# Performance work log

Measured on AMD Instinct MI355X. Metric: run time of the kernel, lower is better.

## Reference

```python
import jax, jax.numpy as jnp
import numpy as np

N_DRUG = 25000
N_DIS = 25000
N = N_DRUG + N_DIS
E = 800000
D_IN = 128
D_OUT = 128


def setup_inputs() -> dict:
    key = jax.random.key(0)
    k1, k2, k3, k4, k5, k6 = jax.random.split(key, 6)
    drug_f = jax.random.normal(k1, (N_DRUG, D_IN), dtype=jnp.float32)
    disease_f = jax.random.normal(k2, (N_DIS, D_IN), dtype=jnp.float32)
    rows = jax.random.randint(k3, (E,), 0, N, dtype=jnp.int64)
    cols = jax.random.randint(k4, (E,), 0, N, dtype=jnp.int64)
    # xavier_uniform_ equivalent for [D_IN, D_OUT]
    limit = float(np.sqrt(6.0 / (D_IN + D_OUT)))
    drug_w = jax.random.uniform(k5, (D_IN, D_OUT), minval=-limit, maxval=limit, dtype=jnp.float32)
    disease_w = jax.random.uniform(k6, (D_IN, D_OUT), minval=-limit, maxval=limit, dtype=jnp.float32)
    return {"drug_f": drug_f, "disease_f": disease_f, "drug_w": drug_w,
            "disease_w": disease_w, "rows": rows, "cols": cols}


def reference(drug_f, disease_f, drug_w, disease_w, rows, cols):
    # per-type linear projection
    drug_h = drug_f @ drug_w          # [n_drug, D_OUT]
    dis_h = disease_f @ disease_w     # [n_dis,  D_OUT]
    node_f = jnp.concatenate([drug_h, dis_h], axis=0)  # [N, D_OUT]
    # row-sum degrees of the (unit-valued) sparse adjacency, clamped at 1
    deg = jax.ops.segment_sum(jnp.ones((rows.shape[0],), node_f.dtype), rows,
                              num_segments=N)
    norm = jnp.clip(deg, 1.0, None) ** -0.5           # [N]
    # symmetric norm: norm * (A @ (norm * x)); SpMM as gather + segment_sum
    node_f = node_f * norm[:, None]
    msgs = node_f[cols]                               # [E, D_OUT]
    node_f = jax.ops.segment_sum(msgs, rows, num_segments=N)
    node_f = node_f * norm[:, None]
    return node_f
```

## Files before the change

kernel.cpp:

```cpp
#include <hip/hip_runtime.h>
#include <hip/hip_bf16.h>

#define D 128
#define CAP 64
#define NSHARD 8
#define NCHUNK 384
#define PART_EDGES 4096

typedef short short8 __attribute__((ext_vector_type(8)));
typedef unsigned short ushort8 __attribute__((ext_vector_type(8)));
typedef float f32x4  __attribute__((ext_vector_type(4)));

__device__ __forceinline__ short f2bf(float x) {
    __hip_bfloat16 b = __float2bfloat16(x);
    return *reinterpret_cast<short*>(&b);
}
__device__ __forceinline__ float bf2f(unsigned short u) {
    return __uint_as_float((unsigned)u << 16);
}

__device__ __forceinline__ void wprep_block(int b16, int tid,
                                            const float* __restrict__ w0,
                                            const float* __restrict__ w1,
                                            __hip_bfloat16* __restrict__ wb) {
    int gid = b16 * 256 + tid;
    int type = gid >> 11;
    int tri  = gid & 2047;
    int lane = tri & 63;
    int ts   = tri >> 6;
    int s = ts & 3, t = ts >> 2;
    const float* W = type ? w1 : w0;
    int n = t * 16 + (lane & 15);
    int kbase = s * 32 + (lane >> 4) * 8;
    short8 v;
    #pragma unroll
    for (int j = 0; j < 8; ++j)
        v[j] = f2bf(W[(size_t)(kbase + j) * D + n]);
    *(short8*)&wb[(size_t)type * 16384 + (size_t)tri * 8] = v;
}

__global__ __launch_bounds__(256) void prep_sort_kernel(const float* __restrict__ w0,
                                                        const float* __restrict__ w1,
                                                        __hip_bfloat16* __restrict__ wb,
                                                        int* __restrict__ bincur, int nbin) {
    int b = blockIdx.x;
    if (b < 16) { wprep_block(b, threadIdx.x, w0, w1, wb); return; }
    int i = threadIdx.x;
    if (i < nbin) bincur[i] = 0;
}

__global__ __launch_bounds__(256) void part_proj_kernel(
    const int* __restrict__ rows, const int* __restrict__ cols,
    int* __restrict__ bincur, unsigned int* __restrict__ payload,
    int E, int nbin, int capbin, int nparts,
    const float* __restrict__ f0, const float* __restrict__ f1,
    const __hip_bfloat16* __restrict__ wb,
    __hip_bfloat16* __restrict__ h,
    int n0, int n1, int nb0) {

    __shared__ short8 Wl[2048];
    int b = blockIdx.x;
    int t = threadIdx.x;

    if (b < nparts) {
        int* hist = (int*)&Wl[0];
        int* base = hist + 256;
        int* cur  = hist + 512;
        int lo = b * PART_EDGES;
        int hi = lo + PART_EDGES; if (hi > E) hi = E;

        hist[t] = 0;
        __syncthreads();
        for (int i = lo + t; i < hi; i += 256)
            atomicAdd(&hist[rows[i] >> 8], 1);
        __syncthreads();
        int c = hist[t];
        base[t] = (t < nbin && c > 0) ? atomicAdd(&bincur[t], c) : 0;
        cur[t] = 0;
        __syncthreads();
        for (int i = lo + t; i < hi; i += 256) {
            int r = rows[i];
            int bn = r >> 8;
            int p = base[bn] + atomicAdd(&cur[bn], 1);
            if (p < capbin)
                payload[(size_t)bn * capbin + p] = ((unsigned)r << 16) | (unsigned)(cols[i] & 0xffff);
        }
        return;
    }

    int pb = b - nparts;
    int type = (pb >= nb0) ? 1 : 0;
    const float* f = type ? f1 : f0;
    int lbase = (type ? (pb - nb0) : pb) * 64;
    int nloc  = type ? n1 : n0;
    int goff  = type ? n0 : 0;

    const short8* src = (const short8*)wb + (size_t)type * 2048;
    for (int i = t; i < 2048; i += 256) Wl[i] = src[i];
    __syncthreads();

    int wave = t >> 6;
    int lane = t & 63;
    int m  = lane & 15;
    int kg = lane >> 4;
    int wrow = lbase + wave * 16;

    int arow = wrow + m;
    int arc = (arow < nloc) ? arow : (nloc - 1);
    const float* fr = f + (size_t)arc * D + kg * 8;
    short8 A[4];
    #pragma unroll
    for (int s = 0; s < 4; ++s) {
        float4 x = *(const float4*)(fr + s * 32);
        float4 y = *(const float4*)(fr + s * 32 + 4);
        short8 a;
        a[0] = f2bf(x.x); a[1] = f2bf(x.y); a[2] = f2bf(x.z); a[3] = f2bf(x.w);
        a[4] = f2bf(y.x); a[5] = f2bf(y.y); a[6] = f2bf(y.z); a[7] = f2bf(y.w);
        A[s] = a;
    }

    #pragma unroll
    for (int tt = 0; tt < 8; ++tt) {
        f32x4 acc = {0.f, 0.f, 0.f, 0.f};
        #pragma unroll
        for (int s = 0; s < 4; ++s)
            acc = __builtin_amdgcn_mfma_f32_16x16x32_bf16(A[s], Wl[(tt * 4 + s) * 64 + lane], acc, 0, 0, 0);
        #pragma unroll
        for (int r = 0; r < 4; ++r) {
            int grow = wrow + kg * 4 + r;
            if (grow < nloc)
                h[(size_t)(goff + grow) * D + tt * 16 + m] = __float2bfloat16(acc[r]);
        }
    }
}

__global__ __launch_bounds__(256) void binfill_kernel(const unsigned int* __restrict__ payload,
                                                      const int* __restrict__ bincur,
                                                      unsigned short* __restrict__ bucket,
                                                      int* __restrict__ cnt,
                                                      float* __restrict__ normf,
                                                      int capbin, int N) {
    __shared__ int rc[256];
    int b = blockIdx.x;
    int t = threadIdx.x;
    rc[t] = 0;
    __syncthreads();
    int cntb = bincur[b]; if (cntb > capbin) cntb = capbin;
    const unsigned int* pp = payload + (size_t)b * capbin;
    for (int i = t; i < cntb; i += 256) {
        unsigned pay = pp[i];
        int rl = (pay >> 16) & 255;
        int p = atomicAdd(&rc[rl], 1);
        if (p < CAP)
            bucket[(size_t)((b << 8) | rl) * CAP + p] = (unsigned short)(pay & 0xffff);
    }
    __syncthreads();
    int r = (b << 8) | t;
    if (r < N) {
        int c = rc[t];
        cnt[r] = c;
        normf[r] = rsqrtf((float)(c < 1 ? 1 : c));
    }
}

__global__ __launch_bounds__(256) void agg_kernel(const int* __restrict__ cnt,
                                                  const float* __restrict__ normf,
                                                  const unsigned short* __restrict__ bucket,
                                                  const __hip_bfloat16* __restrict__ h,
                                                  float* __restrict__ out, int n) {
    int wave = threadIdx.x >> 6;
    int lane = threadIdx.x & 63;
    int r = blockIdx.x * 4 + wave;
    if (r >= n) return;
    int d = cnt[r]; if (d > CAP) d = CAP;
    int s = r * CAP;
    int g  = lane >> 4;
    int sl = lane & 15;

    float acc[8] = {0.f,0.f,0.f,0.f,0.f,0.f,0.f,0.f};
    for (int j = 0; j < d; j += 8) {
        int j0 = j + g, j1 = j + 4 + g;
        bool v0 = j0 < d, v1 = j1 < d;
        int c0 = bucket[s + (v0 ? j0 : 0)];
        int c1 = bucket[s + (v1 ? j1 : 0)];
        float w0 = v0 ? normf[c0] : 0.f;
        float w1 = v1 ? normf[c1] : 0.f;
        ushort8 a = *(const ushort8*)&h[(size_t)c0 * D + sl * 8];
        ushort8 bb = *(const ushort8*)&h[(size_t)c1 * D + sl * 8];
        #pragma unroll
        for (int k = 0; k < 8; ++k)
            acc[k] += w0 * bf2f(a[k]) + w1 * bf2f(bb[k]);
    }
    #pragma unroll
    for (int k = 0; k < 8; ++k) {
        acc[k] += __shfl_xor(acc[k], 16);
        acc[k] += __shfl_xor(acc[k], 32);
    }
    if (g == 0) {
        float nr = normf[r];
        float* po = &out[(size_t)r * D + sl * 8];
        float4 o0 = make_float4(acc[0]*nr, acc[1]*nr, acc[2]*nr, acc[3]*nr);
        float4 o1 = make_float4(acc[4]*nr, acc[5]*nr, acc[6]*nr, acc[7]*nr);
        *(float4*)po = o0;
        *(float4*)(po + 4) = o1;
    }
}

__global__ __launch_bounds__(256) void prep_kernel(const float* __restrict__ w0,
                                                   const float* __restrict__ w1,
                                                   __hip_bfloat16* __restrict__ wb,
                                                   int* __restrict__ cnt, int N) {
    int b = blockIdx.x;
    if (b < 16) { wprep_block(b, threadIdx.x, w0, w1, wb); }
    else {
        int i = (b - 16) * 256 + threadIdx.x;
        if (i < N) cnt[i] = 0;
    }
}

__global__ __launch_bounds__(256) void fill_shard_kernel(const int* __restrict__ rows,
                                                         const int* __restrict__ cols,
                                                         int* __restrict__ cnt,
                                                         unsigned short* __restrict__ bucket,
                                                         int E, int shsz, int ch) {
    int s     = blockIdx.x & (NSHARD - 1);
    int chunk = blockIdx.x >> 3;
    int lo = chunk * ch;
    int hi = lo + ch; if (hi > E) hi = E;
    int rlo = s * shsz;
    for (int i = lo + (int)threadIdx.x; i < hi; i += 256) {
        int r = rows[i];
        if ((unsigned)(r - rlo) < (unsigned)shsz) {
            int p = atomicAdd(&cnt[r], 1);
            if (p < CAP) bucket[(size_t)r * CAP + p] = (unsigned short)cols[i];
        }
    }
}

__global__ void norm_from_cnt_kernel(const int* __restrict__ cnt, float* __restrict__ normf, int N) {
    int i = blockIdx.x * 256 + threadIdx.x;
    if (i < N) { int c = cnt[i]; normf[i] = rsqrtf((float)(c < 1 ? 1 : c)); }
}

extern "C" void kernel_launch(void* const* d_in, const int* in_sizes, int n_in,
                              void* d_out, int out_size, void* d_ws, size_t ws_size,
                              hipStream_t stream) {
    const float* drug_f    = (const float*)d_in[0];
    const float* disease_f = (const float*)d_in[1];
    const float* drug_w    = (const float*)d_in[2];
    const float* disease_w = (const float*)d_in[3];
    const int*   rows      = (const int*)d_in[4];
    const int*   cols      = (const int*)d_in[5];
    float* out = (float*)d_out;

    int n_drug = in_sizes[0] / D;
    int n_dis  = in_sizes[1] / D;
    int N = n_drug + n_dis;
    int E = in_sizes[4];
    (void)out_size; (void)n_in;

    char* ws = (char*)d_ws;
    size_t off = 0;
    auto alloc = [&](size_t bytes) { void* p = ws + off; off = (off + bytes + 255) & ~(size_t)255; return p; };

    int*            cnt      = (int*)alloc(sizeof(int) * N);
    float*          normf    = (float*)alloc(sizeof(float) * N);
    __hip_bfloat16* h_raw    = (__hip_bfloat16*)alloc(sizeof(__hip_bfloat16) * (size_t)N * D);
    __hip_bfloat16* wb       = (__hip_bfloat16*)alloc(sizeof(__hip_bfloat16) * 2 * 16384);
    unsigned short* bucket   = (unsigned short*)alloc((size_t)N * CAP * sizeof(unsigned short));

    int nb0 = (n_drug + 63) / 64;
    int nb1 = (n_dis + 63) / 64;

    int nbin   = (N + 255) >> 8;
    int capbin = (((E / nbin) * 3 / 2) + 63) & ~63;
    size_t sort_need = off
        + ((sizeof(int) * nbin + 255) & ~(size_t)255)
        + ((sizeof(unsigned int) * (size_t)nbin * capbin + 255) & ~(size_t)255);

    if (ws_size >= sort_need && nbin <= 256) {
        int*          bincur  = (int*)alloc(sizeof(int) * nbin);
        unsigned int* payload = (unsigned int*)alloc(sizeof(unsigned int) * (size_t)nbin * capbin);

        int nparts = (E + PART_EDGES - 1) / PART_EDGES;
        prep_sort_kernel<<<17, 256, 0, stream>>>(drug_w, disease_w, wb, bincur, nbin);
        part_proj_kernel<<<nparts + nb0 + nb1, 256, 0, stream>>>(
            rows, cols, bincur, payload, E, nbin, capbin, nparts,
            drug_f, disease_f, wb, h_raw, n_drug, n_dis, nb0);
        binfill_kernel<<<nbin, 256, 0, stream>>>(payload, bincur, bucket, cnt, normf, capbin, N);
        agg_kernel<<<(N + 3) / 4, 256, 0, stream>>>(cnt, normf, bucket, h_raw, out, N);
    } else {
        int shsz = (N + NSHARD - 1) / NSHARD;
        int ch   = (E + NCHUNK - 1) / NCHUNK;
        int prep_blocks = 16 + (N + 255) / 256;

        prep_kernel<<<prep_blocks, 256, 0, stream>>>(drug_w, disease_w, wb, cnt, N);
        fill_shard_kernel<<<NCHUNK * NSHARD, 256, 0, stream>>>(rows, cols, cnt, bucket, E, shsz, ch);
        norm_from_cnt_kernel<<<(N + 255) / 256, 256, 0, stream>>>(cnt, normf, N);
        part_proj_kernel<<<nb0 + nb1, 256, 0, stream>>>(
            rows, cols, (int*)nullptr, (unsigned int*)nullptr, E, nbin, capbin, 0,
            drug_f, disease_f, wb, h_raw, n_drug, n_dis, nb0);
        agg_kernel<<<(N + 3) / 4, 256, 0, stream>>>(cnt, normf, bucket, h_raw, out, N);
    }
}
```

Measured before the change: 78.26 us.

## Halve sort bin width and preload bucket columns per lane in aggregation

Bins in the edge partition/binfill pass now cover 128 rows instead of 256. This doubles the bin count, so binfill runs about twice as many blocks for better GPU occupancy, and the partition kernel's histogram loops are generalised beyond 256 bins. The aggregation kernel now loads each row's column list and neighbour norms once per lane, then broadcasts them with shuffles. It handles one edge per 16-lane group per iteration instead of two, which removes the repeated bucket and norm loads but leaves fewer gathers in flight per iteration.

Result: faster. 71.17 us (-9.1%).

```diff
diff --git a/kernel.cpp b/kernel.cpp
--- a/kernel.cpp
+++ b/kernel.cpp
@@ -3,6 +3,7 @@
 
 #define D 128
 #define CAP 64
+#define BINSH 7
 #define NSHARD 8
 #define NCHUNK 384
 #define PART_EDGES 4096
@@ -45,8 +46,7 @@
                                                         int* __restrict__ bincur, int nbin) {
     int b = blockIdx.x;
     if (b < 16) { wprep_block(b, threadIdx.x, w0, w1, wb); return; }
-    int i = threadIdx.x;
-    if (i < nbin) bincur[i] = 0;
+    for (int i = threadIdx.x; i < nbin; i += 256) bincur[i] = 0;
 }
 
 __global__ __launch_bounds__(256) void part_proj_kernel(
@@ -64,23 +64,25 @@
 
     if (b < nparts) {
         int* hist = (int*)&Wl[0];
-        int* base = hist + 256;
-        int* cur  = hist + 512;
+        int* base = hist + 512;
+        int* cur  = hist + 1024;
         int lo = b * PART_EDGES;
         int hi = lo + PART_EDGES; if (hi > E) hi = E;
 
-        hist[t] = 0;
+        for (int i = t; i < nbin; i += 256) hist[i] = 0;
         __syncthreads();
         for (int i = lo + t; i < hi; i += 256)
-            atomicAdd(&hist[rows[i] >> 8], 1);
+            atomicAdd(&hist[rows[i] >> BINSH], 1);
         __syncthreads();
-        int c = hist[t];
-        base[t] = (t < nbin && c > 0) ? atomicAdd(&bincur[t], c) : 0;
-        cur[t] = 0;
+        for (int i = t; i < nbin; i += 256) {
+            int c = hist[i];
+            base[i] = (c > 0) ? atomicAdd(&bincur[i], c) : 0;
+            cur[i] = 0;
+        }
         __syncthreads();
         for (int i = lo + t; i < hi; i += 256) {
             int r = rows[i];
-            int bn = r >> 8;
+            int bn = r >> BINSH;
             int p = base[bn] + atomicAdd(&cur[bn], 1);
             if (p < capbin)
                 payload[(size_t)bn * capbin + p] = ((unsigned)r << 16) | (unsigned)(cols[i] & 0xffff);
@@ -140,26 +142,28 @@
                                                       int* __restrict__ cnt,
                                                       float* __restrict__ normf,
                                                       int capbin, int N) {
-    __shared__ int rc[256];
+    __shared__ int rc[128];
     int b = blockIdx.x;
     int t = threadIdx.x;
-    rc[t] = 0;
+    if (t < 128) rc[t] = 0;
     __syncthreads();
     int cntb = bincur[b]; if (cntb > capbin) cntb = capbin;
     const unsigned int* pp = payload + (size_t)b * capbin;
     for (int i = t; i < cntb; i += 256) {
         unsigned pay = pp[i];
-        int rl = (pay >> 16) & 255;
+        int rl = (pay >> 16) & 127;
         int p = atomicAdd(&rc[rl], 1);
         if (p < CAP)
-            bucket[(size_t)((b << 8) | rl) * CAP + p] = (unsigned short)(pay & 0xffff);
+            bucket[(size_t)((b << BINSH) | rl) * CAP + p] = (unsigned short)(pay & 0xffff);
     }
     __syncthreads();
-    int r = (b << 8) | t;
-    if (r < N) {
-        int c = rc[t];
-        cnt[r] = c;
-        normf[r] = rsqrtf((float)(c < 1 ? 1 : c));
+    if (t < 128) {
+        int r = (b << BINSH) | t;
+        if (r < N) {
+            int c = rc[t];
+            cnt[r] = c;
+            normf[r] = rsqrtf((float)(c < 1 ? 1 : c));
+        }
     }
 }
 
@@ -174,22 +178,23 @@
     if (r >= n) return;
     int d = cnt[r]; if (d > CAP) d = CAP;
     int s = r * CAP;
+
+    int col = (int)bucket[s + lane];
+    int cs  = (lane < d) ? col : 0;
+    float wl = (lane < d) ? normf[cs] : 0.f;
+
     int g  = lane >> 4;
     int sl = lane & 15;
 
     float acc[8] = {0.f,0.f,0.f,0.f,0.f,0.f,0.f,0.f};
-    for (int j = 0; j < d; j += 8) {
-        int j0 = j + g, j1 = j + 4 + g;
-        bool v0 = j0 < d, v1 = j1 < d;
-        int c0 = bucket[s + (v0 ? j0 : 0)];
-        int c1 = bucket[s + (v1 ? j1 : 0)];
-        float w0 = v0 ? normf[c0] : 0.f;
-        float w1 = v1 ? normf[c1] : 0.f;
-        ushort8 a = *(const ushort8*)&h[(size_t)c0 * D + sl * 8];
-        ushort8 bb = *(const ushort8*)&h[(size_t)c1 * D + sl * 8];
+    for (int j = 0; j < d; j += 4) {
+        int e = j + g;
+        float we = __shfl(wl, e & 63); if (e >= d) we = 0.f;
+        int   ce = __shfl(cs, e & 63);
+        ushort8 v = *(const ushort8*)&h[(size_t)ce * D + sl * 8];
         #pragma unroll
         for (int k = 0; k < 8; ++k)
-            acc[k] += w0 * bf2f(a[k]) + w1 * bf2f(bb[k]);
+            acc[k] += we * bf2f(v[k]);
     }
     #pragma unroll
     for (int k = 0; k < 8; ++k) {
@@ -199,10 +204,8 @@
     if (g == 0) {
         float nr = normf[r];
         float* po = &out[(size_t)r * D + sl * 8];
-        float4 o0 = make_float4(acc[0]*nr, acc[1]*nr, acc[2]*nr, acc[3]*nr);
-        float4 o1 = make_float4(acc[4]*nr, acc[5]*nr, acc[6]*nr, acc[7]*nr);
-        *(float4*)po = o0;
-        *(float4*)(po + 4) = o1;
+        *(float4*)po       = make_float4(acc[0]*nr, acc[1]*nr, acc[2]*nr, acc[3]*nr);
+        *(float4*)(po + 4) = make_float4(acc[4]*nr, acc[5]*nr, acc[6]*nr, acc[7]*nr);
     }
 }
 
@@ -272,13 +275,13 @@
     int nb0 = (n_drug + 63) / 64;
     int nb1 = (n_dis + 63) / 64;
 
-    int nbin   = (N + 255) >> 8;
+    int nbin   = (N + (1 << BINSH) - 1) >> BINSH;
     int capbin = (((E / nbin) * 3 / 2) + 63) & ~63;
     size_t sort_need = off
         + ((sizeof(int) * nbin + 255) & ~(size_t)255)
         + ((sizeof(unsigned int) * (size_t)nbin * capbin + 255) & ~(size_t)255);
 
-    if (ws_size >= sort_need && nbin <= 256) {
+    if (ws_size >= sort_need && nbin <= 512) {
         int*          bincur  = (int*)alloc(sizeof(int) * nbin);
         unsigned int* payload = (unsigned int*)alloc(sizeof(unsigned int) * (size_t)nbin * capbin);
 
```
